# Optimization experiments

Hardware: AMD Instinct MI355X
Metric: run time of the kernel (lower is better)

The kernel has to match this reference:

```python
import jax, jax.numpy as jnp
import numpy as np

N_NODES = 20000
N_EDGES = 640000
IN_DIM = 8
DIMS = [IN_DIM, IN_DIM * 3, IN_DIM * 8, IN_DIM * 16, IN_DIM * 32]  # 8,24,64,128,256
P = 512   # number of pathways (len(pathway))
S = 64    # nodes per pathway subgraph
D = DIMS[-1]  # Set2Set input dim = 256
H1, H2 = 256, 64


def setup_inputs() -> dict:
    key = jax.random.key(0)
    ks = iter(jax.random.split(key, 64))
    inp = {}
    inp['h'] = jax.random.normal(next(ks), (N_NODES, IN_DIM), jnp.float32)
    inp['src'] = jax.random.randint(next(ks), (N_EDGES,), 0, N_NODES, jnp.int32)
    inp['dst'] = jax.random.randint(next(ks), (N_EDGES,), 0, N_NODES, jnp.int32)
    inp['path_nodes'] = jax.random.randint(next(ks), (P, S), 0, N_NODES, jnp.int32)
    sc = 0.05
    # GIN MLP (torch Linear: weight [out,in])
    for i in range(4):
        inp[f'W{i+1}'] = sc * jax.random.normal(next(ks), (DIMS[i+1], DIMS[i]), jnp.float32)
        inp[f'b{i+1}'] = jnp.zeros((DIMS[i+1],), jnp.float32)
    # 3 Set2Set modules, each an LSTM(input=2D, hidden=D), PyTorch gate layout [i,f,g,o]
    inp['s2s_Wih'] = sc * jax.random.normal(next(ks), (3, 4 * D, 2 * D), jnp.float32)
    inp['s2s_Whh'] = sc * jax.random.normal(next(ks), (3, 4 * D, D), jnp.float32)
    inp['s2s_bih'] = jnp.zeros((3, 4 * D), jnp.float32)
    inp['s2s_bhh'] = jnp.zeros((3, 4 * D), jnp.float32)
    inp['Wg'] = sc * jax.random.normal(next(ks), (1, 2 * D * 3), jnp.float32)
    inp['bg'] = jnp.zeros((1,), jnp.float32)
    inp['Wl1'] = sc * jax.random.normal(next(ks), (H1, P), jnp.float32)
    inp['bl1'] = jnp.zeros((H1,), jnp.float32)
    inp['Wl2'] = sc * jax.random.normal(next(ks), (H2, H1), jnp.float32)
    inp['bl2'] = jnp.zeros((H2,), jnp.float32)
    inp['Wl3'] = sc * jax.random.normal(next(ks), (1, H2), jnp.float32)
    inp['bl3'] = jnp.zeros((1,), jnp.float32)
    return inp


def _set2set(x, Wih, Whh, bih, bhh):
    """Set2Set pooling, n_iters=2, 1 LSTM layer. x: [P, S, D] -> [P, 2D]."""
    p, s, d = x.shape
    q_star = jnp.zeros((p, 2 * d), x.dtype)
    hs = jnp.zeros((p, d), x.dtype)
    cs = jnp.zeros((p, d), x.dtype)
    for _ in range(2):
        gates = q_star @ Wih.T + hs @ Whh.T + bih + bhh  # [p, 4d]
        i, f, g, o = jnp.split(gates, 4, axis=-1)
        cs = jax.nn.sigmoid(f) * cs + jax.nn.sigmoid(i) * jnp.tanh(g)
        hs = jax.nn.sigmoid(o) * jnp.tanh(cs)
        q = hs  # [p, d]
        alpha = jax.nn.softmax(jnp.einsum('psd,pd->ps', x, q), axis=1)
        r = jnp.einsum('ps,psd->pd', alpha, x)
        q_star = jnp.concatenate([q, r], axis=-1)
    return q_star


def reference(h, src, dst, path_nodes,
              W1, b1, W2, b2, W3, b3, W4, b4,
              s2s_Wih, s2s_Whh, s2s_bih, s2s_bhh,
              Wg, bg, Wl1, bl1, Wl2, bl2, Wl3, bl3):
    n = h.shape[0]
    for W, b in ((W1, b1), (W2, b2), (W3, b3), (W4, b4)):
        agg = jax.ops.segment_sum(h[src], dst, num_segments=n)
        h = jax.nn.relu((h + agg) @ W.T + b)
    # pathway subgraph extraction + batched Set2Set readouts
    x = h[path_nodes]  # [P, S, D]
    reads = [_set2set(x, s2s_Wih[k], s2s_Whh[k], s2s_bih[k], s2s_bhh[k]) for k in range(3)]
    readout = jnp.stack(reads, axis=1).reshape(x.shape[0], -1)  # [P, 6D]
    xg = readout @ Wg.T + bg  # [P, 1]
    z = xg.reshape(1, -1)     # [1, P]
    z = jnp.tanh(z @ Wl1.T + bl1)   # dropout omitted (eval/deterministic)
    z = jax.nn.relu(z @ Wl2.T + bl2)
    return jax.nn.sigmoid(z @ Wl3.T + bl3)  # [1, 1]
```

## Files before the change

kernel.cpp:

```cpp
#include <hip/hip_runtime.h>
#include <hip/hip_bf16.h>
#include <math.h>

#define N_NODES 20000
#define N_EDGES 640000
#define P_PATH 512
#define BIN_CAP 96
#define CNT_STRIDE 32
#define NTILES64 313

typedef __attribute__((ext_vector_type(8))) short bf16x8;
typedef __attribute__((ext_vector_type(4))) float f32x4;

static __device__ __forceinline__ unsigned short f2bf(float f) {
    unsigned int b = __float_as_uint(f);
    unsigned int r = (b + 0x7fffu + ((b >> 16) & 1u)) >> 16;
    return (unsigned short)r;
}
static __device__ __forceinline__ float bfl(unsigned int u) { return __uint_as_float(u << 16); }
static __device__ __forceinline__ float bfh(unsigned int u) { return __uint_as_float(u & 0xffff0000u); }
static __device__ __forceinline__ void bf16_acc(float4& acc, uint2 u) {
    acc.x += bfl(u.x); acc.y += bfh(u.x);
    acc.z += bfl(u.y); acc.w += bfh(u.y);
}
static __device__ __forceinline__ float sigm(float x) { return 1.f / (1.f + expf(-x)); }

__global__ __launch_bounds__(256) void init_all(const float* __restrict__ W2,
                                                const float* __restrict__ W3f,
                                                const float* __restrict__ W4f,
                                                const float* __restrict__ Wihf,
                                                int* __restrict__ counts,
                                                unsigned short* __restrict__ Wb2p,
                                                unsigned short* __restrict__ Wb3,
                                                unsigned short* __restrict__ Wb4,
                                                unsigned short* __restrict__ Wihb) {
    int i = blockIdx.x * 256 + threadIdx.x;
    if (i < N_NODES * CNT_STRIDE) counts[i] = 0;
    if (i < 2048) {
        int r = i >> 5, c = i & 31;
        Wb2p[i] = (c < 24) ? f2bf(W2[r * 24 + c]) : (unsigned short)0;
    }
    if (i < 8192) Wb3[i] = f2bf(W3f[i]);
    if (i < 32768) Wb4[i] = f2bf(W4f[i]);
    {
        int m = i >> 18;
        int rem = i & 262143;
        int j = rem >> 8, k = rem & 255;
        Wihb[i] = f2bf(Wihf[((size_t)m * 1024 + j) * 512 + 256 + k]);
    }
}

__global__ __launch_bounds__(256) void fill_bins(const int* __restrict__ src,
                                                 const int* __restrict__ dst,
                                                 int* __restrict__ counts,
                                                 unsigned short* __restrict__ bins, int n) {
    int e = blockIdx.x * 256 + threadIdx.x;
    if (e < n) {
        int node = dst[e];
        int pos = atomicAdd(&counts[node * CNT_STRIDE], 1);
        if (pos < BIN_CAP) bins[(size_t)node * BIN_CAP + pos] = (unsigned short)src[e];
    }
}

__global__ __launch_bounds__(256) void gin_l1(const float* __restrict__ h0,
                                              const int* __restrict__ counts,
                                              const unsigned short* __restrict__ bins,
                                              const float* __restrict__ W1,
                                              const float* __restrict__ b1,
                                              unsigned short* __restrict__ shA32) {
    __shared__ float XL1[64 * 8];
    int tid = threadIdx.x;
    int node0 = blockIdx.x * 64;
    float4* Xf = reinterpret_cast<float4*>(XL1);
    const float4* hp = reinterpret_cast<const float4*>(h0);
    for (int it = tid; it < 128; it += 256) {
        int nl = it >> 1, d4 = it & 1;
        int node = node0 + nl;
        float4 a = {0.f, 0.f, 0.f, 0.f};
        if (node < N_NODES) {
            a = hp[(size_t)node * 2 + d4];
            int cnt = counts[node * CNT_STRIDE];
            if (cnt > BIN_CAP) cnt = BIN_CAP;
            const unsigned short* bp = bins + (size_t)node * BIN_CAP;
            int e = 0;
            for (; e + 4 <= cnt; e += 4) {
                float4 v0 = hp[(size_t)bp[e] * 2 + d4];
                float4 v1 = hp[(size_t)bp[e + 1] * 2 + d4];
                float4 v2 = hp[(size_t)bp[e + 2] * 2 + d4];
                float4 v3 = hp[(size_t)bp[e + 3] * 2 + d4];
                a.x += v0.x + v1.x + v2.x + v3.x;
                a.y += v0.y + v1.y + v2.y + v3.y;
                a.z += v0.z + v1.z + v2.z + v3.z;
                a.w += v0.w + v1.w + v2.w + v3.w;
            }
            for (; e < cnt; ++e) {
                float4 v = hp[(size_t)bp[e] * 2 + d4];
                a.x += v.x; a.y += v.y; a.z += v.z; a.w += v.w;
            }
        }
        Xf[it] = a;
    }
    __syncthreads();
    int nl = tid >> 2, jg = tid & 3;
    int node = node0 + nl;
    if (node < N_NODES) {
        const float* Xa = XL1 + nl * 8;
#pragma unroll
        for (int jj = 0; jj < 6; ++jj) {
            int j = jg * 6 + jj;
            float acc = b1[j];
#pragma unroll
            for (int k = 0; k < 8; ++k) acc += W1[j * 8 + k] * Xa[k];
            shA32[(size_t)node * 32 + j] = f2bf(fmaxf(acc, 0.f));
        }
        shA32[(size_t)node * 32 + 24 + jg * 2] = 0;
        shA32[(size_t)node * 32 + 25 + jg * 2] = 0;
    }
}

template <int NODES, int TPN, int UPT, int K, int N>
__global__ __launch_bounds__(256) void gin_layer2(const unsigned short* __restrict__ hb_in,
                                                  const int* __restrict__ counts,
                                                  const unsigned short* __restrict__ bins,
                                                  const unsigned short* __restrict__ Wb,
                                                  const float* __restrict__ bias,
                                                  unsigned short* __restrict__ out_bf) {
    constexpr int D4 = TPN * UPT;
    static_assert(D4 * 4 == K, "K mismatch");
    __shared__ unsigned short X[NODES * K];
    int tid = threadIdx.x;
    int node0 = blockIdx.x * NODES;
    const uint2* hp = reinterpret_cast<const uint2*>(hb_in);
    uint2* Xp = reinterpret_cast<uint2*>(X);
    {
        int nl = tid / TPN;
        int sub = tid - nl * TPN;
        int d4b = sub * UPT;
        int node = node0 + nl;
        float4 acc[UPT];
#pragma unroll
        for (int u = 0; u < UPT; ++u) acc[u] = {0.f, 0.f, 0.f, 0.f};
        if (node < N_NODES) {
            const uint2* selfp = hp + (size_t)node * D4 + d4b;
#pragma unroll
            for (int u = 0; u < UPT; ++u) bf16_acc(acc[u], selfp[u]);
            int cnt = counts[node * CNT_STRIDE];
            if (cnt > BIN_CAP) cnt = BIN_CAP;
            const unsigned short* bp = bins + (size_t)node * BIN_CAP;
            int e = 0;
            for (; e + 4 <= cnt; e += 4) {
                const uint2* r0 = hp + (size_t)bp[e] * D4 + d4b;
                const uint2* r1 = hp + (size_t)bp[e + 1] * D4 + d4b;
                const uint2* r2 = hp + (size_t)bp[e + 2] * D4 + d4b;
                const uint2* r3 = hp + (size_t)bp[e + 3] * D4 + d4b;
                uint2 t0[UPT], t1[UPT], t2[UPT], t3[UPT];
#pragma unroll
                for (int u = 0; u < UPT; ++u) {
                    t0[u] = r0[u]; t1[u] = r1[u]; t2[u] = r2[u]; t3[u] = r3[u];
                }
#pragma unroll
                for (int u = 0; u < UPT; ++u) {
                    bf16_acc(acc[u], t0[u]); bf16_acc(acc[u], t1[u]);
                    bf16_acc(acc[u], t2[u]); bf16_acc(acc[u], t3[u]);
                }
            }
            for (; e < cnt; ++e) {
                const uint2* r0 = hp + (size_t)bp[e] * D4 + d4b;
#pragma unroll
                for (int u = 0; u < UPT; ++u) bf16_acc(acc[u], r0[u]);
            }
        }
#pragma unroll
        for (int u = 0; u < UPT; ++u) {
            uint2 o;
            o.x = (unsigned)f2bf(acc[u].x) | ((unsigned)f2bf(acc[u].y) << 16);
            o.y = (unsigned)f2bf(acc[u].z) | ((unsigned)f2bf(acc[u].w) << 16);
            Xp[nl * D4 + d4b + u] = o;
        }
    }
    __syncthreads();
    constexpr int R = NODES / 16;
    constexpr int C = 4 / R;
    constexpr int NT = N / 16 / C;
    constexpr int KC = K / 32;
    int ln = tid & 63, wv = tid >> 6;
    int rg = wv % R, cg = wv / R;
    int lr = ln & 15, lk = ln >> 4;
    int colbase = cg * (N / C);
    f32x4 acc[NT];
#pragma unroll
    for (int t = 0; t < NT; ++t) acc[t] = (f32x4){0.f, 0.f, 0.f, 0.f};
#pragma unroll
    for (int kc = 0; kc < KC; ++kc) {
        bf16x8 a = *reinterpret_cast<const bf16x8*>(&X[(rg * 16 + lr) * K + kc * 32 + lk * 8]);
#pragma unroll
        for (int t = 0; t < NT; ++t) {
            bf16x8 b = *reinterpret_cast<const bf16x8*>(
                &Wb[(size_t)(colbase + t * 16 + lr) * K + kc * 32 + lk * 8]);
            acc[t] = __builtin_amdgcn_mfma_f32_16x16x32_bf16(a, b, acc[t], 0, 0, 0);
        }
    }
#pragma unroll
    for (int t = 0; t < NT; ++t) {
        float bj = bias[colbase + t * 16 + lr];
#pragma unroll
        for (int r = 0; r < 4; ++r) {
            int row = node0 + rg * 16 + lk * 4 + r;
            if (row < N_NODES)
                out_bf[(size_t)row * N + colbase + t * 16 + lr] =
                    f2bf(fmaxf(acc[t][r] + bj, 0.f));
        }
    }
}

__global__ __launch_bounds__(256) void attn1_cpart(const unsigned short* __restrict__ h4b,
                                                   const int* __restrict__ path,
                                                   const float* __restrict__ Wih,
                                                   const float* __restrict__ Whh,
                                                   const float* __restrict__ bih,
                                                   const float* __restrict__ bhh,
                                                   unsigned short* __restrict__ r0b,
                                                   float* __restrict__ cpart_all) {
    int p = blockIdx.x;
    __shared__ unsigned short xs[64 * 256];
    __shared__ float qs[3][256];
    __shared__ float al[3][64];
    __shared__ int nodes[64];
    int tid = threadIdx.x;
    int ln = tid & 63, wv = tid >> 6;
#pragma unroll
    for (int m = 0; m < 3; ++m) {
        const float* bi = bih + (size_t)m * 1024;
        const float* bh = bhh + (size_t)m * 1024;
        float gi = bi[tid] + bh[tid];
        float gg = bi[512 + tid] + bh[512 + tid];
        float go = bi[768 + tid] + bh[768 + tid];
        qs[m][tid] = sigm(go) * tanhf(sigm(gi) * tanhf(gg));
    }
    if (tid < 64) nodes[tid] = path[p * 64 + tid];
    __syncthreads();
    const uint2* h4p = reinterpret_cast<const uint2*>(h4b);
    for (int s = wv; s < 64; s += 4) {
        uint2 u = h4p[(size_t)nodes[s] * 64 + ln];
        *reinterpret_cast<uint2*>(&xs[s * 256 + ln * 4]) = u;
        float v0 = bfl(u.x), v1 = bfh(u.x), v2 = bfl(u.y), v3 = bfh(u.y);
        float d0 = v0 * qs[0][ln * 4] + v1 * qs[0][ln * 4 + 1] +
                   v2 * qs[0][ln * 4 + 2] + v3 * qs[0][ln * 4 + 3];
        float d1 = v0 * qs[1][ln * 4] + v1 * qs[1][ln * 4 + 1] +
                   v2 * qs[1][ln * 4 + 2] + v3 * qs[1][ln * 4 + 3];
        float d2 = v0 * qs[2][ln * 4] + v1 * qs[2][ln * 4 + 1] +
                   v2 * qs[2][ln * 4 + 2] + v3 * qs[2][ln * 4 + 3];
        for (int off = 32; off >= 1; off >>= 1) {
            d0 += __shfl_xor(d0, off, 64);
            d1 += __shfl_xor(d1, off, 64);
            d2 += __shfl_xor(d2, off, 64);
        }
        if (ln == 0) { al[0][s] = d0; al[1][s] = d1; al[2][s] = d2; }
    }
    __syncthreads();
    if (wv < 3) {
        float v = al[wv][ln];
        float mx = v;
        for (int off = 32; off >= 1; off >>= 1) mx = fmaxf(mx, __shfl_xor(mx, off, 64));
        float e = expf(v - mx);
        float s = e;
        for (int off = 32; off >= 1; off >>= 1) s += __shfl_xor(s, off, 64);
        al[wv][ln] = e / s;
    }
    __syncthreads();
    float a0 = 0.f, a1 = 0.f, a2 = 0.f;
    for (int s = 0; s < 64; ++s) {
        float xv = bfl((unsigned)xs[s * 256 + tid]);
        a0 += al[0][s] * xv;
        a1 += al[1][s] * xv;
        a2 += al[2][s] * xv;
    }
    r0b[((size_t)0 * P_PATH + p) * 256 + tid] = f2bf(a0);
    r0b[((size_t)1 * P_PATH + p) * 256 + tid] = f2bf(a1);
    r0b[((size_t)2 * P_PATH + p) * 256 + tid] = f2bf(a2);
#pragma unroll
    for (int rep = 0; rep < 2; ++rep) {
        int qi = wv + rep * 4;
        if (qi < 6) {
            int o = p * 6 + qi;
            int m = o >> 10, j = o & 1023;
            float4 wiv = reinterpret_cast<const float4*>(Wih + ((size_t)m * 1024 + j) * 512)[ln];
            float4 whv = reinterpret_cast<const float4*>(Whh + ((size_t)m * 1024 + j) * 256)[ln];
            float4 hv = *reinterpret_cast<const float4*>(&qs[m][ln * 4]);
            float acc = hv.x * (wiv.x + whv.x) + hv.y * (wiv.y + whv.y) +
                        hv.z * (wiv.z + whv.z) + hv.w * (wiv.w + whv.w);
            for (int off = 32; off >= 1; off >>= 1) acc += __shfl_xor(acc, off, 64);
            if (ln == 0) cpart_all[o] = acc + bih[o] + bhh[o];
        }
    }
}

__global__ __launch_bounds__(256) void mfma_gates(const unsigned short* __restrict__ r0b,
                                                  const unsigned short* __restrict__ Wihb,
                                                  const float* __restrict__ cpart_all,
                                                  float* __restrict__ gates_all) {
    int m = blockIdx.z;
    int p0 = blockIdx.x * 64;
    int j0 = blockIdx.y * 64;
    const unsigned short* A = r0b + (size_t)m * 512 * 256;
    const unsigned short* B = Wihb + (size_t)m * 1024 * 256 + (size_t)j0 * 256;
    const float* bias = cpart_all + m * 1024 + j0;
    float* og = gates_all + (size_t)m * 512 * 1024;
    int tid = threadIdx.x;
    int ln = tid & 63, wv = tid >> 6;
    int lr = ln & 15, lk = ln >> 4;
    int row0 = p0 + wv * 16;
    f32x4 acc[4];
#pragma unroll
    for (int t = 0; t < 4; ++t) acc[t] = (f32x4){0.f, 0.f, 0.f, 0.f};
#pragma unroll
    for (int kc = 0; kc < 8; ++kc) {
        bf16x8 a = *reinterpret_cast<const bf16x8*>(&A[(size_t)(row0 + lr) * 256 + kc * 32 + lk * 8]);
#pragma unroll
        for (int t = 0; t < 4; ++t) {
            bf16x8 b = *reinterpret_cast<const bf16x8*>(&B[(size_t)(t * 16 + lr) * 256 + kc * 32 + lk * 8]);
            acc[t] = __builtin_amdgcn_mfma_f32_16x16x32_bf16(a, b, acc[t], 0, 0, 0);
        }
    }
#pragma unroll
    for (int t = 0; t < 4; ++t) {
        float bj = bias[t * 16 + lr];
#pragma unroll
        for (int rr = 0; rr < 4; ++rr) {
            int row = row0 + lk * 4 + rr;
            og[(size_t)row * 1024 + j0 + t * 16 + lr] = acc[t][rr] + bj;
        }
    }
}

__global__ __launch_bounds__(256) void attn2(const unsigned short* __restrict__ h4b,
                                             const int* __restrict__ path,
                                             const float* __restrict__ gates_all,
                                             const float* __restrict__ bih,
                                             const float* __restrict__ bhh,
                                             const float* __restrict__ Wg,
                                             const float* __restrict__ bg,
                                             float* __restrict__ xg) {
    int p = blockIdx.x;
    __shared__ unsigned short xs[64 * 256];
    __shared__ float qs[3][256];
    __shared__ float al[3][64];
    __shared__ float wsum[4];
    __shared__ int nodes[64];
    int tid = threadIdx.x;
    int ln = tid & 63, wv = tid >> 6;
#pragma unroll
    for (int m = 0; m < 3; ++m) {
        const float* bi = bih + (size_t)m * 1024;
        const float* bh = bhh + (size_t)m * 1024;
        float gi0 = bi[tid] + bh[tid];
        float gg0 = bi[512 + tid] + bh[512 + tid];
        float c0 = sigm(gi0) * tanhf(gg0);
        const float* g = gates_all + ((size_t)m * P_PATH + p) * 1024;
        float gi = g[tid], gf = g[256 + tid], gg = g[512 + tid], go = g[768 + tid];
        float c1 = sigm(gf) * c0 + sigm(gi) * tanhf(gg);
        qs[m][tid] = sigm(go) * tanhf(c1);
    }
    if (tid < 64) nodes[tid] = path[p * 64 + tid];
    __syncthreads();
    const uint2* h4p = reinterpret_cast<const uint2*>(h4b);
    for (int s = wv; s < 64; s += 4) {
        uint2 u = h4p[(size_t)nodes[s] * 64 + ln];
        *reinterpret_cast<uint2*>(&xs[s * 256 + ln * 4]) = u;
        float v0 = bfl(u.x), v1 = bfh(u.x), v2 = bfl(u.y), v3 = bfh(u.y);
        float d0 = v0 * qs[0][ln * 4] + v1 * qs[0][ln * 4 + 1] +
                   v2 * qs[0][ln * 4 + 2] + v3 * qs[0][ln * 4 + 3];
        float d1 = v0 * qs[1][ln * 4] + v1 * qs[1][ln * 4 + 1] +
                   v2 * qs[1][ln * 4 + 2] + v3 * qs[1][ln * 4 + 3];
        float d2 = v0 * qs[2][ln * 4] + v1 * qs[2][ln * 4 + 1] +
                   v2 * qs[2][ln * 4 + 2] + v3 * qs[2][ln * 4 + 3];
        for (int off = 32; off >= 1; off >>= 1) {
            d0 += __shfl_xor(d0, off, 64);
            d1 += __shfl_xor(d1, off, 64);
            d2 += __shfl_xor(d2, off, 64);
        }
        if (ln == 0) { al[0][s] = d0; al[1][s] = d1; al[2][s] = d2; }
    }
    __syncthreads();
    if (wv < 3) {
        float v = al[wv][ln];
        float mx = v;
        for (int off = 32; off >= 1; off >>= 1) mx = fmaxf(mx, __shfl_xor(mx, off, 64));
        float e = expf(v - mx);
        float s = e;
        for (int off = 32; off >= 1; off >>= 1) s += __shfl_xor(s, off, 64);
        al[wv][ln] = e / s;
    }
    __syncthreads();
    float a0 = 0.f, a1 = 0.f, a2 = 0.f;
    for (int s = 0; s < 64; ++s) {
        float xv = bfl((unsigned)xs[s * 256 + tid]);
        a0 += al[0][s] * xv;
        a1 += al[1][s] * xv;
        a2 += al[2][s] * xv;
    }
    float part = qs[0][tid] * Wg[tid] + a0 * Wg[256 + tid] +
                 qs[1][tid] * Wg[512 + tid] + a1 * Wg[768 + tid] +
                 qs[2][tid] * Wg[1024 + tid] + a2 * Wg[1280 + tid];
    for (int off = 32; off >= 1; off >>= 1) part += __shfl_xor(part, off, 64);
    if (ln == 0) wsum[wv] = part;
    __syncthreads();
    if (tid == 0) xg[p] = wsum[0] + wsum[1] + wsum[2] + wsum[3] + bg[0];
}

__global__ __launch_bounds__(256) void final_mlp(const float* __restrict__ xg,
                                                 const float* __restrict__ Wl1,
                                                 const float* __restrict__ bl1,
                                                 const float* __restrict__ Wl2,
                                                 const float* __restrict__ bl2,
                                                 const float* __restrict__ Wl3,
                                                 const float* __restrict__ bl3,
                                                 float* __restrict__ out) {
    __shared__ float z[512];
    __shared__ float z1[256];
    __shared__ float z2[64];
    int t = threadIdx.x;
    z[t] = xg[t];
    z[256 + t] = xg[256 + t];
    __syncthreads();
    float acc = bl1[t];
    const float* w = Wl1 + (size_t)t * 512;
    for (int k = 0; k < 512; ++k) acc += w[k] * z[k];
    z1[t] = tanhf(acc);
    __syncthreads();
    if (t < 64) {
        float a = bl2[t];
        const float* w2 = Wl2 + (size_t)t * 256;
        for (int k = 0; k < 256; ++k) a += w2[k] * z1[k];
        z2[t] = fmaxf(a, 0.f);
    }
    __syncthreads();
    if (t < 64) {
        float v = Wl3[t] * z2[t];
        for (int off = 32; off >= 1; off >>= 1) v += __shfl_xor(v, off, 64);
        if (t == 0) out[0] = 1.f / (1.f + expf(-(v + bl3[0])));
    }
}

extern "C" void kernel_launch(void* const* d_in, const int* in_sizes, int n_in,
                              void* d_out, int out_size, void* d_ws, size_t ws_size,
                              hipStream_t stream) {
    const float* h0 = (const float*)d_in[0];
    const int* src = (const int*)d_in[1];
    const int* dst = (const int*)d_in[2];
    const int* path = (const int*)d_in[3];
    const float* W1 = (const float*)d_in[4];
    const float* b1 = (const float*)d_in[5];
    const float* W2 = (const float*)d_in[6];
    const float* b2 = (const float*)d_in[7];
    const float* W3 = (const float*)d_in[8];
    const float* b3 = (const float*)d_in[9];
    const float* W4 = (const float*)d_in[10];
    const float* b4 = (const float*)d_in[11];
    const float* Wih = (const float*)d_in[12];
    const float* Whh = (const float*)d_in[13];
    const float* bih = (const float*)d_in[14];
    const float* bhh = (const float*)d_in[15];
    const float* Wg = (const float*)d_in[16];
    const float* bg = (const float*)d_in[17];
    const float* Wl1 = (const float*)d_in[18];
    const float* bl1 = (const float*)d_in[19];
    const float* Wl2 = (const float*)d_in[20];
    const float* bl2 = (const float*)d_in[21];
    const float* Wl3 = (const float*)d_in[22];
    const float* bl3 = (const float*)d_in[23];

    char* ws = (char*)d_ws;
    int* counts = (int*)(ws + 0);
    unsigned short* bins = (unsigned short*)(ws + 2621440);
    unsigned short* shA32 = (unsigned short*)(ws + 6553600);
    unsigned short* shB64 = (unsigned short*)(ws + 7864320);
    unsigned short* shA128 = (unsigned short*)(ws + 10485760);
    unsigned short* h4b = (unsigned short*)(ws + 15728640);
    unsigned short* r0b = (unsigned short*)(ws + 26214400);
    float* gates_all = (float*)(ws + 27000832);
    float* cpart_all = (float*)(ws + 33292288);
    float* xg = (float*)(ws + 33357824);
    unsigned short* Wb2p = (unsigned short*)(ws + 33423360);
    unsigned short* Wb3 = (unsigned short*)(ws + 33488896);
    unsigned short* Wb4 = (unsigned short*)(ws + 33554432);
    unsigned short* Wihb = (unsigned short*)(ws + 33619968);

    init_all<<<3072, 256, 0, stream>>>(W2, W3, W4, Wih, counts, Wb2p, Wb3, Wb4, Wihb);
    fill_bins<<<(N_EDGES + 255) / 256, 256, 0, stream>>>(src, dst, counts, bins, N_EDGES);

    gin_l1<<<NTILES64, 256, 0, stream>>>(h0, counts, bins, W1, b1, shA32);
    gin_layer2<32, 8, 1, 32, 64><<<625, 256, 0, stream>>>(shA32, counts, bins, Wb2p, b2, shB64);
    gin_layer2<16, 16, 1, 64, 128><<<1250, 256, 0, stream>>>(shB64, counts, bins, Wb3, b3, shA128);
    gin_layer2<16, 16, 2, 128, 256><<<1250, 256, 0, stream>>>(shA128, counts, bins, Wb4, b4, h4b);

    attn1_cpart<<<P_PATH, 256, 0, stream>>>(h4b, path, Wih, Whh, bih, bhh, r0b, cpart_all);
    mfma_gates<<<dim3(8, 16, 3), 256, 0, stream>>>(r0b, Wihb, cpart_all, gates_all);
    attn2<<<P_PATH, 256, 0, stream>>>(h4b, path, gates_all, bih, bhh, Wg, bg, xg);
    final_mlp<<<1, 256, 0, stream>>>(xg, Wl1, bl1, Wl2, bl2, Wl3, bl3, (float*)d_out);
}
```

Baseline: 274.3 us.

## Split layer-1 gather across threads, vectorize bin reads, use bf16 Wl1

Layer-1 aggregation now uses all 256 threads: each node's edge list is split into two halves handled by separate threads, and the halves are summed in shared memory. The GIN gather loops now load 8 bin indices at once with a 16-byte load and issue 8 row gathers per iteration, giving more memory-level parallelism. The final MLP reads a bf16 copy of Wl1 that init_all produces, halving the bytes that single block streams. The costs are more registers in the gather loop, a possibly misaligned uint4 bin load (bins stride 96 shorts keeps it aligned), and reduced precision for Wl1.

```diff
diff --git a/kernel.cpp b/kernel.cpp
--- a/kernel.cpp
+++ b/kernel.cpp
@@ -29,11 +29,13 @@
                                                 const float* __restrict__ W3f,
                                                 const float* __restrict__ W4f,
                                                 const float* __restrict__ Wihf,
+                                                const float* __restrict__ Wl1f,
                                                 int* __restrict__ counts,
                                                 unsigned short* __restrict__ Wb2p,
                                                 unsigned short* __restrict__ Wb3,
                                                 unsigned short* __restrict__ Wb4,
-                                                unsigned short* __restrict__ Wihb) {
+                                                unsigned short* __restrict__ Wihb,
+                                                unsigned short* __restrict__ Wl1b) {
     int i = blockIdx.x * 256 + threadIdx.x;
     if (i < N_NODES * CNT_STRIDE) counts[i] = 0;
     if (i < 2048) {
@@ -42,6 +44,7 @@
     }
     if (i < 8192) Wb3[i] = f2bf(W3f[i]);
     if (i < 32768) Wb4[i] = f2bf(W4f[i]);
+    if (i < 131072) Wl1b[i] = f2bf(Wl1f[i]);
     {
         int m = i >> 18;
         int rem = i & 262143;
@@ -68,22 +71,28 @@
                                               const float* __restrict__ W1,
                                               const float* __restrict__ b1,
                                               unsigned short* __restrict__ shA32) {
-    __shared__ float XL1[64 * 8];
+    __shared__ float4 XP[64][2][2];
     int tid = threadIdx.x;
     int node0 = blockIdx.x * 64;
-    float4* Xf = reinterpret_cast<float4*>(XL1);
     const float4* hp = reinterpret_cast<const float4*>(h0);
-    for (int it = tid; it < 128; it += 256) {
-        int nl = it >> 1, d4 = it & 1;
+    {
+        int nl = tid >> 2;
+        int d4 = (tid >> 1) & 1;
+        int half = tid & 1;
         int node = node0 + nl;
         float4 a = {0.f, 0.f, 0.f, 0.f};
         if (node < N_NODES) {
-            a = hp[(size_t)node * 2 + d4];
             int cnt = counts[node * CNT_STRIDE];
             if (cnt > BIN_CAP) cnt = BIN_CAP;
+            int lo = half ? (cnt >> 1) : 0;
+            int hi = half ? cnt : (cnt >> 1);
+            if (!half) {
+                float4 s = hp[(size_t)node * 2 + d4];
+                a.x += s.x; a.y += s.y; a.z += s.z; a.w += s.w;
+            }
             const unsigned short* bp = bins + (size_t)node * BIN_CAP;
-            int e = 0;
-            for (; e + 4 <= cnt; e += 4) {
+            int e = lo;
+            for (; e + 4 <= hi; e += 4) {
                 float4 v0 = hp[(size_t)bp[e] * 2 + d4];
                 float4 v1 = hp[(size_t)bp[e + 1] * 2 + d4];
                 float4 v2 = hp[(size_t)bp[e + 2] * 2 + d4];
@@ -93,24 +102,30 @@
                 a.z += v0.z + v1.z + v2.z + v3.z;
                 a.w += v0.w + v1.w + v2.w + v3.w;
             }
-            for (; e < cnt; ++e) {
+            for (; e < hi; ++e) {
                 float4 v = hp[(size_t)bp[e] * 2 + d4];
                 a.x += v.x; a.y += v.y; a.z += v.z; a.w += v.w;
             }
         }
-        Xf[it] = a;
+        XP[nl][half][d4] = a;
     }
     __syncthreads();
     int nl = tid >> 2, jg = tid & 3;
     int node = node0 + nl;
     if (node < N_NODES) {
-        const float* Xa = XL1 + nl * 8;
+        float4 x0a = XP[nl][0][0], x0b = XP[nl][1][0];
+        float4 x1a = XP[nl][0][1], x1b = XP[nl][1][1];
+        float x[8];
+        x[0] = x0a.x + x0b.x; x[1] = x0a.y + x0b.y;
+        x[2] = x0a.z + x0b.z; x[3] = x0a.w + x0b.w;
+        x[4] = x1a.x + x1b.x; x[5] = x1a.y + x1b.y;
+        x[6] = x1a.z + x1b.z; x[7] = x1a.w + x1b.w;
 #pragma unroll
         for (int jj = 0; jj < 6; ++jj) {
             int j = jg * 6 + jj;
             float acc = b1[j];
 #pragma unroll
-            for (int k = 0; k < 8; ++k) acc += W1[j * 8 + k] * Xa[k];
+            for (int k = 0; k < 8; ++k) acc += W1[j * 8 + k] * x[k];
             shA32[(size_t)node * 32 + j] = f2bf(fmaxf(acc, 0.f));
         }
         shA32[(size_t)node * 32 + 24 + jg * 2] = 0;
@@ -148,20 +163,33 @@
             if (cnt > BIN_CAP) cnt = BIN_CAP;
             const unsigned short* bp = bins + (size_t)node * BIN_CAP;
             int e = 0;
-            for (; e + 4 <= cnt; e += 4) {
-                const uint2* r0 = hp + (size_t)bp[e] * D4 + d4b;
-                const uint2* r1 = hp + (size_t)bp[e + 1] * D4 + d4b;
-                const uint2* r2 = hp + (size_t)bp[e + 2] * D4 + d4b;
-                const uint2* r3 = hp + (size_t)bp[e + 3] * D4 + d4b;
+            for (; e + 8 <= cnt; e += 8) {
+                uint4 bv = *reinterpret_cast<const uint4*>(bp + e);
+                int s0 = bv.x & 0xffff, s1 = bv.x >> 16;
+                int s2 = bv.y & 0xffff, s3 = bv.y >> 16;
+                int s4 = bv.z & 0xffff, s5 = bv.z >> 16;
+                int s6 = bv.w & 0xffff, s7 = bv.w >> 16;
+                const uint2* r0 = hp + (size_t)s0 * D4 + d4b;
+                const uint2* r1 = hp + (size_t)s1 * D4 + d4b;
+                const uint2* r2 = hp + (size_t)s2 * D4 + d4b;
+                const uint2* r3 = hp + (size_t)s3 * D4 + d4b;
+                const uint2* r4 = hp + (size_t)s4 * D4 + d4b;
+                const uint2* r5 = hp + (size_t)s5 * D4 + d4b;
+                const uint2* r6 = hp + (size_t)s6 * D4 + d4b;
+                const uint2* r7 = hp + (size_t)s7 * D4 + d4b;
                 uint2 t0[UPT], t1[UPT], t2[UPT], t3[UPT];
+                uint2 t4[UPT], t5[UPT], t6[UPT], t7[UPT];
 #pragma unroll
                 for (int u = 0; u < UPT; ++u) {
                     t0[u] = r0[u]; t1[u] = r1[u]; t2[u] = r2[u]; t3[u] = r3[u];
+                    t4[u] = r4[u]; t5[u] = r5[u]; t6[u] = r6[u]; t7[u] = r7[u];
                 }
 #pragma unroll
                 for (int u = 0; u < UPT; ++u) {
                     bf16_acc(acc[u], t0[u]); bf16_acc(acc[u], t1[u]);
                     bf16_acc(acc[u], t2[u]); bf16_acc(acc[u], t3[u]);
+                    bf16_acc(acc[u], t4[u]); bf16_acc(acc[u], t5[u]);
+                    bf16_acc(acc[u], t6[u]); bf16_acc(acc[u], t7[u]);
                 }
             }
             for (; e < cnt; ++e) {
@@ -409,7 +437,7 @@
 }
 
 __global__ __launch_bounds__(256) void final_mlp(const float* __restrict__ xg,
-                                                 const float* __restrict__ Wl1,
+                                                 const unsigned short* __restrict__ Wl1b,
                                                  const float* __restrict__ bl1,
                                                  const float* __restrict__ Wl2,
                                                  const float* __restrict__ bl2,
@@ -424,8 +452,12 @@
     z[256 + t] = xg[256 + t];
     __syncthreads();
     float acc = bl1[t];
-    const float* w = Wl1 + (size_t)t * 512;
-    for (int k = 0; k < 512; ++k) acc += w[k] * z[k];
+    const uint2* w = reinterpret_cast<const uint2*>(Wl1b + (size_t)t * 512);
+    for (int k = 0; k < 128; ++k) {
+        uint2 u = w[k];
+        acc += bfl(u.x) * z[k * 4] + bfh(u.x) * z[k * 4 + 1] +
+               bfl(u.y) * z[k * 4 + 2] + bfh(u.y) * z[k * 4 + 3];
+    }
     z1[t] = tanhf(acc);
     __syncthreads();
     if (t < 64) {
@@ -485,8 +517,9 @@
     unsigned short* Wb3 = (unsigned short*)(ws + 33488896);
     unsigned short* Wb4 = (unsigned short*)(ws + 33554432);
     unsigned short* Wihb = (unsigned short*)(ws + 33619968);
-
-    init_all<<<3072, 256, 0, stream>>>(W2, W3, W4, Wih, counts, Wb2p, Wb3, Wb4, Wihb);
+    unsigned short* Wl1b = (unsigned short*)(ws + 35192832);
+
+    init_all<<<3072, 256, 0, stream>>>(W2, W3, W4, Wih, Wl1, counts, Wb2p, Wb3, Wb4, Wihb, Wl1b);
     fill_bins<<<(N_EDGES + 255) / 256, 256, 0, stream>>>(src, dst, counts, bins, N_EDGES);
 
     gin_l1<<<NTILES64, 256, 0, stream>>>(h0, counts, bins, W1, b1, shA32);
@@ -497,5 +530,5 @@
     attn1_cpart<<<P_PATH, 256, 0, stream>>>(h4b, path, Wih, Whh, bih, bhh, r0b, cpart_all);
     mfma_gates<<<dim3(8, 16, 3), 256, 0, stream>>>(r0b, Wihb, cpart_all, gates_all);
     attn2<<<P_PATH, 256, 0, stream>>>(h4b, path, gates_all, bih, bhh, Wg, bg, xg);
-    final_mlp<<<1, 256, 0, stream>>>(xg, Wl1, bl1, Wl2, bl2, Wl3, bl3, (float*)d_out);
-}
+    final_mlp<<<1, 256, 0, stream>>>(xg, Wl1b, bl1, Wl2, bl2, Wl3, bl3, (float*)d_out);
+}
```

Result: faster. 262.0 us (-4.5%).
